# Kernel optimization log

Measured on AMD Instinct MI355X. Metric: run time of the kernel, lower is better.

## Reference

```python
import jax, jax.numpy as jnp
import numpy as np

B, T, IN, H, L = 32, 1024, 256, 256, 2  # batch, length, input_size, hidden_size, num_layers


def _lstm_scan(x, W_ih, W_hh, b_ih, b_hh, reverse):
    """Single-direction LSTM over time. x:[B,T,D] -> h:[B,T,H]. PyTorch gate order i,f,g,o."""
    b, t, _ = x.shape
    h_dim = W_hh.shape[1]
    # Precompute input contribution for all timesteps at once: [T,B,4H]
    xg = (jnp.einsum('btd,gd->btg', x, W_ih) + b_ih + b_hh).transpose(1, 0, 2)

    def step(carry, g_t):
        h, c = carry
        g = g_t + h @ W_hh.T
        i, f, gg, o = jnp.split(g, 4, axis=-1)
        c = jax.nn.sigmoid(f) * c + jax.nn.sigmoid(i) * jnp.tanh(gg)
        h = jax.nn.sigmoid(o) * jnp.tanh(c)
        return (h, c), h

    init = (jnp.zeros((b, h_dim), x.dtype), jnp.zeros((b, h_dim), x.dtype))
    _, hs = jax.lax.scan(step, init, xg, reverse=reverse)  # hs:[T,B,H], original time order
    return hs.transpose(1, 0, 2)


def setup_inputs() -> dict:
    key = jax.random.key(0)
    ks = iter(jax.random.split(key, 40))
    s = 1.0 / np.sqrt(H)
    inp = {'x': jax.random.normal(next(ks), (B, T, IN), jnp.float32)}
    for l in range(L):
        d_in = IN if l == 0 else 2 * H
        for dr in ('f', 'r'):
            inp[f'W_ih_{dr}{l}'] = jax.random.uniform(next(ks), (4 * H, d_in), jnp.float32, -s, s)
            inp[f'W_hh_{dr}{l}'] = jax.random.uniform(next(ks), (4 * H, H), jnp.float32, -s, s)
            inp[f'b_ih_{dr}{l}'] = jax.random.uniform(next(ks), (4 * H,), jnp.float32, -s, s)
            inp[f'b_hh_{dr}{l}'] = jax.random.uniform(next(ks), (4 * H,), jnp.float32, -s, s)
    return inp


def reference(x,
              W_ih_f0, W_hh_f0, b_ih_f0, b_hh_f0,
              W_ih_r0, W_hh_r0, b_ih_r0, b_hh_r0,
              W_ih_f1, W_hh_f1, b_ih_f1, b_hh_f1,
              W_ih_r1, W_hh_r1, b_ih_r1, b_hh_r1):
    fwd = [(W_ih_f0, W_hh_f0, b_ih_f0, b_hh_f0), (W_ih_f1, W_hh_f1, b_ih_f1, b_hh_f1)]
    rev = [(W_ih_r0, W_hh_r0, b_ih_r0, b_hh_r0), (W_ih_r1, W_hh_r1, b_ih_r1, b_hh_r1)]
    h = x
    for l in range(L):
        hf = _lstm_scan(h, *fwd[l], reverse=False)
        hr = _lstm_scan(h, *rev[l], reverse=True)
        h = jnp.concatenate([hf, hr], axis=-1)  # [B,T,2H]
    return h
```

## Files before the change

kernel.cpp:

```cpp
#include <hip/hip_runtime.h>
#include <hip/hip_fp16.h>


#define T_LEN 1024
#define BATCH 32
#define HID   256
#define G4    1024

struct __align__(16) Half8 { __half h[8]; };

typedef _Float16 f16x2 __attribute__((ext_vector_type(2)));
typedef _Float16 half8_t __attribute__((ext_vector_type(8)));
typedef float f32x4 __attribute__((ext_vector_type(4)));

__device__ __forceinline__ f16x2 pack_f16x2(float lo, float hi) {
    f16x2 r; r.x = (_Float16)lo; r.y = (_Float16)hi; return r;
}
__device__ __forceinline__ float dot2acc(f16x2 a, f16x2 b, float c) {
#if __has_builtin(__builtin_amdgcn_fdot2)
    return __builtin_amdgcn_fdot2(a, b, c, false);
#else
    return c + (float)a.x * (float)b.x + (float)a.y * (float)b.y;
#endif
}

template <int CTRL>
__device__ __forceinline__ unsigned qperm_u32(unsigned v) {
    int r = __builtin_amdgcn_update_dpp((int)v, (int)v, CTRL, 0xF, 0xF, true);
    return (unsigned)r;
}

__device__ __forceinline__ float sigm(float x) { return 1.0f / (1.0f + __expf(-x)); }
__device__ __forceinline__ float tanh_fast(float x) {
    float e = __expf(2.f * x);
    return 1.f - 2.f / (e + 1.f);
}

__global__ __launch_bounds__(256, 2) void proj_mfma(
    const float* __restrict__ A, int K,
    const float* __restrict__ Wf, const float* __restrict__ Wr,
    const float* __restrict__ bih_f, const float* __restrict__ bhh_f,
    const float* __restrict__ bih_r, const float* __restrict__ bhh_r,
    __half* __restrict__ xg)
{
    const int dir = blockIdx.z;
    const float* __restrict__ W   = dir ? Wr    : Wf;
    const float* __restrict__ bih = dir ? bih_r : bih_f;
    const float* __restrict__ bhh = dir ? bhh_r : bhh_f;
    __half* __restrict__ outp = xg + (size_t)dir * ((size_t)BATCH * T_LEN * G4);

    __shared__ char psm[36864];
    __half* As = (__half*)psm;
    __half* Bs = (__half*)(psm + 18432);

    const int tid  = threadIdx.x;
    const int lane = tid & 63;
    const int wave = tid >> 6;
    const int wm   = wave >> 1;
    const int wn   = wave & 1;
    const int fr   = lane & 15;
    const int fk   = lane >> 4;
    const int m0   = blockIdx.y * 128;
    const int n0   = blockIdx.x * 128;

    float biasv[4];
    #pragma unroll
    for (int ni = 0; ni < 4; ++ni) {
        int n = n0 + wn * 64 + ni * 16 + fr;
        biasv[ni] = bih[n] + bhh[n];
    }

    f32x4 acc[4][4];
    #pragma unroll
    for (int mi = 0; mi < 4; ++mi)
        #pragma unroll
        for (int ni = 0; ni < 4; ++ni)
            acc[mi][ni] = (f32x4){0.f, 0.f, 0.f, 0.f};

    for (int k0 = 0; k0 < K; k0 += 64) {
        #pragma unroll
        for (int it = 0; it < 4; ++it) {
            int t2  = tid + it * 256;
            int row = t2 >> 3;
            int ks  = (t2 & 7) * 8;
            const float* pa = &A[(size_t)(m0 + row) * K + k0 + ks];
            const float* pb = &W[(size_t)(n0 + row) * K + k0 + ks];
            float4 a0 = *reinterpret_cast<const float4*>(pa);
            float4 a1 = *reinterpret_cast<const float4*>(pa + 4);
            float4 b0 = *reinterpret_cast<const float4*>(pb);
            float4 b1 = *reinterpret_cast<const float4*>(pb + 4);
            Half8 ha, hb;
            ha.h[0] = __float2half(a0.x); ha.h[1] = __float2half(a0.y);
            ha.h[2] = __float2half(a0.z); ha.h[3] = __float2half(a0.w);
            ha.h[4] = __float2half(a1.x); ha.h[5] = __float2half(a1.y);
            ha.h[6] = __float2half(a1.z); ha.h[7] = __float2half(a1.w);
            hb.h[0] = __float2half(b0.x); hb.h[1] = __float2half(b0.y);
            hb.h[2] = __float2half(b0.z); hb.h[3] = __float2half(b0.w);
            hb.h[4] = __float2half(b1.x); hb.h[5] = __float2half(b1.y);
            hb.h[6] = __float2half(b1.z); hb.h[7] = __float2half(b1.w);
            *reinterpret_cast<Half8*>(&As[row * 72 + ks]) = ha;
            *reinterpret_cast<Half8*>(&Bs[row * 72 + ks]) = hb;
        }
        __syncthreads();

        #pragma unroll
        for (int kk = 0; kk < 2; ++kk) {
            half8_t af[4], bf[4];
            #pragma unroll
            for (int mi = 0; mi < 4; ++mi)
                af[mi] = *reinterpret_cast<const half8_t*>(
                    &As[(wm * 64 + mi * 16 + fr) * 72 + kk * 32 + fk * 8]);
            #pragma unroll
            for (int ni = 0; ni < 4; ++ni)
                bf[ni] = *reinterpret_cast<const half8_t*>(
                    &Bs[(wn * 64 + ni * 16 + fr) * 72 + kk * 32 + fk * 8]);
            #pragma unroll
            for (int mi = 0; mi < 4; ++mi)
                #pragma unroll
                for (int ni = 0; ni < 4; ++ni)
                    acc[mi][ni] = __builtin_amdgcn_mfma_f32_16x16x32_f16(
                        af[mi], bf[ni], acc[mi][ni], 0, 0, 0);
        }
        __syncthreads();
    }

    __half* Cs = (__half*)psm;
    #pragma unroll
    for (int mi = 0; mi < 4; ++mi)
        #pragma unroll
        for (int ni = 0; ni < 4; ++ni) {
            #pragma unroll
            for (int i = 0; i < 4; ++i) {
                int row = wm * 64 + mi * 16 + fk * 4 + i;
                int col = wn * 64 + ni * 16 + fr;
                Cs[row * 136 + col] = __float2half(acc[mi][ni][i] + biasv[ni]);
            }
        }
    __syncthreads();
    #pragma unroll
    for (int it = 0; it < 8; ++it) {
        int slot = it * 256 + tid;
        int row  = slot >> 4;
        int c8   = (slot & 15) * 8;
        Half8 v = *reinterpret_cast<const Half8*>(&Cs[row * 136 + c8]);
        *reinterpret_cast<Half8*>(&outp[(size_t)(m0 + row) * G4 + n0 + c8]) = v;
    }
}

extern "C" __global__ __launch_bounds__(512, 2) void recur12_kernel(
    const __half* __restrict__ xg,
    const float* __restrict__ Whh_f,
    const float* __restrict__ Whh_r,
    float* __restrict__ outp,
    unsigned long long* __restrict__ hbt,
    unsigned int tagbase)
{
    __shared__ char smem[55296];
    __half* hl  = (__half*)smem;
    float*  scr = (float*)(smem + 1024);

    const int tid = threadIdx.x;
    const int bid = blockIdx.x;
    const int jq  = bid >> 6;
    const int d   = (bid >> 5) & 1;
    const int b   = bid & 31;
    const float* __restrict__ Whh = d ? Whh_r : Whh_f;

    const int kh = tid >> 8;
    const int r  = tid & 255;
    const int q  = r >> 6;
    const int jl = r & 63;
    const int n_my = (q << 8) + jq * 64 + jl;

    unsigned wh[64];
    {
        const float* wrow = Whh + (size_t)n_my * HID + kh * 128;
        #pragma unroll
        for (int i = 0; i < 32; ++i) {
            float4 w4 = *reinterpret_cast<const float4*>(&wrow[i * 4]);
            wh[2 * i]     = __builtin_bit_cast(unsigned, pack_f16x2(w4.x, w4.y));
            wh[2 * i + 1] = __builtin_bit_cast(unsigned, pack_f16x2(w4.z, w4.w));
        }
    }
    #pragma unroll
    for (int i = 0; i < 64; ++i) asm volatile("" : "+v"(wh[i]));

    unsigned long long* hb = hbt + (size_t)(d * 32 + b) * 512;

    if (tid < 32) {
        __hip_atomic_store(&hb[256 + jq * 32 + tid],
                           (unsigned long long)tagbase << 32,
                           __ATOMIC_RELAXED, __HIP_MEMORY_SCOPE_AGENT);
    }
    if (tid < 64) hl[0 * 256 + jq * 64 + tid] = __float2half(0.f);

    const bool isPoll = (tid >= 256) && (tid < 352);
    int pslot = 0, pdst = 0;
    if (isPoll) {
        int u  = tid - 256;
        int fq = u >> 5;
        int qq = fq + (fq >= jq);
        int pi = u & 31;
        pslot  = qq * 32 + pi;
        pdst   = qq * 64 + pi * 2;
    }

    const __half* __restrict__ xgp =
        xg + ((size_t)(d * BATCH + b)) * T_LEN * G4 + n_my;

    float c_state = 0.f;

    for (int st = 0; st < T_LEN; ++st) {
        const int t = d ? (T_LEN - 1 - st) : st;

        float xv = (kh == 0) ? __half2float(xgp[(size_t)t * G4]) : 0.f;

        __half* hlcur = hl + (st & 1) * 256;

        if (isPoll) {
            const unsigned int exp = tagbase + (unsigned)st;
            unsigned long long* src = hb + (size_t)((st + 1) & 1) * 256 + pslot;
            unsigned long long v =
                __hip_atomic_load(src, __ATOMIC_RELAXED, __HIP_MEMORY_SCOPE_AGENT);
            while ((unsigned int)(v >> 32) != exp)
                v = __hip_atomic_load(src, __ATOMIC_RELAXED, __HIP_MEMORY_SCOPE_AGENT);
            *reinterpret_cast<unsigned*>(&hlcur[pdst]) = (unsigned)v;
        }
        __syncthreads();

        float a0 = xv, a1 = 0.f;
        {
            const float4* hp = reinterpret_cast<const float4*>(hlcur + kh * 128);
            #pragma unroll
            for (int i = 0; i < 16; ++i) {
                float4 hv = hp[i];
                a0 = dot2acc(__builtin_bit_cast(f16x2, hv.x), __builtin_bit_cast(f16x2, wh[4 * i + 0]), a0);
                a1 = dot2acc(__builtin_bit_cast(f16x2, hv.y), __builtin_bit_cast(f16x2, wh[4 * i + 1]), a1);
                a0 = dot2acc(__builtin_bit_cast(f16x2, hv.z), __builtin_bit_cast(f16x2, wh[4 * i + 2]), a0);
                a1 = dot2acc(__builtin_bit_cast(f16x2, hv.w), __builtin_bit_cast(f16x2, wh[4 * i + 3]), a1);
            }
        }
        scr[kh * 256 + r] = a0 + a1;
        __syncthreads();

        if (tid < 64) {
            float gi = scr[      tid] + scr[256 +       tid];
            float gf = scr[ 64 + tid] + scr[256 +  64 + tid];
            float gg = scr[128 + tid] + scr[256 + 128 + tid];
            float go = scr[192 + tid] + scr[256 + 192 + tid];
            float ii = sigm(gi);
            float ff = sigm(gf);
            float g2 = tanh_fast(gg);
            float oo = sigm(go);
            c_state = ff * c_state + ii * g2;
            float h = oo * tanh_fast(c_state);
            const int j = jq * 64 + tid;

            __half h16 = __float2half(h);
            hl[((st + 1) & 1) * 256 + j] = h16;

            unsigned hbits = (unsigned)__builtin_bit_cast(unsigned short, h16);
            unsigned nb = qperm_u32<0xB1>(hbits);
            if ((tid & 1) == 0) {
                unsigned payload = hbits | (nb << 16);
                unsigned long long pv =
                    ((unsigned long long)(tagbase + (unsigned)st + 1u) << 32) | payload;
                __hip_atomic_store(&hb[(size_t)(st & 1) * 256 + jq * 32 + (tid >> 1)], pv,
                                   __ATOMIC_RELAXED, __HIP_MEMORY_SCOPE_AGENT);
            }
            outp[((size_t)b * T_LEN + t) * (2 * HID) + d * HID + j] = h;
        }
    }
}

extern "C" void kernel_launch(void* const* d_in, const int* in_sizes, int n_in,
                              void* d_out, int out_size, void* d_ws, size_t ws_size,
                              hipStream_t stream)
{
    const float* x       = (const float*)d_in[0];
    const float* W_ih_f0 = (const float*)d_in[1];
    const float* W_hh_f0 = (const float*)d_in[2];
    const float* b_ih_f0 = (const float*)d_in[3];
    const float* b_hh_f0 = (const float*)d_in[4];
    const float* W_ih_r0 = (const float*)d_in[5];
    const float* W_hh_r0 = (const float*)d_in[6];
    const float* b_ih_r0 = (const float*)d_in[7];
    const float* b_hh_r0 = (const float*)d_in[8];
    const float* W_ih_f1 = (const float*)d_in[9];
    const float* W_hh_f1 = (const float*)d_in[10];
    const float* b_ih_f1 = (const float*)d_in[11];
    const float* b_hh_f1 = (const float*)d_in[12];
    const float* W_ih_r1 = (const float*)d_in[13];
    const float* W_hh_r1 = (const float*)d_in[14];
    const float* b_ih_r1 = (const float*)d_in[15];
    const float* b_hh_r1 = (const float*)d_in[16];

    float* outp = (float*)d_out;

    __half* xg = (__half*)d_ws;
    const size_t xg_bytes = (size_t)2 * BATCH * T_LEN * G4 * sizeof(__half);
    unsigned long long* hbt = (unsigned long long*)((char*)d_ws + xg_bytes);

    hipMemsetAsync(hbt, 0, 262144, stream);

    proj_mfma<<<dim3(8, 256, 2), 256, 0, stream>>>(x, 256, W_ih_f0, W_ih_r0,
        b_ih_f0, b_hh_f0, b_ih_r0, b_hh_r0, xg);
    {
        const __half* xg_c = xg;
        unsigned int base0 = 1u;
        void* args[] = {(void*)&xg_c, (void*)&W_hh_f0, (void*)&W_hh_r0,
                        (void*)&outp, (void*)&hbt, (void*)&base0};
        hipLaunchCooperativeKernel(reinterpret_cast<const void*>(recur12_kernel),
                                   dim3(256), dim3(512), args, 0, stream);
    }

    proj_mfma<<<dim3(8, 256, 2), 256, 0, stream>>>(outp, 512, W_ih_f1, W_ih_r1,
        b_ih_f1, b_hh_f1, b_ih_r1, b_hh_r1, xg);
    {
        const __half* xg_c = xg;
        unsigned int base1 = 4096u;
        void* args[] = {(void*)&xg_c, (void*)&W_hh_f1, (void*)&W_hh_r1,
                        (void*)&outp, (void*)&hbt, (void*)&base1};
        hipLaunchCooperativeKernel(reinterpret_cast<const void*>(recur12_kernel),
                                   dim3(256), dim3(512), args, 0, stream);
    }
}
```

Measured before the change: 2.923 ms.

## Interleave gate rows per cell and combine gates via DPP to drop a barrier

Restructures the recurrent kernel so each of 256 compute threads holds a full 256-wide W_hh row (128 packed registers), with the four gates of a cell in adjacent lanes. The gates are exchanged with DPP quad permutes instead of going through an LDS scratch buffer, which removes the second __syncthreads per timestep and the split-K reduction. The block shrinks to 384 threads: 256 compute plus poll threads, with compute given raised priority. It also requests 96KB of dynamic LDS, apparently to force one block per CU, at the cost of much higher register pressure per thread.

```diff
diff --git a/kernel.cpp b/kernel.cpp
--- a/kernel.cpp
+++ b/kernel.cpp
@@ -25,9 +25,10 @@
 }
 
 template <int CTRL>
-__device__ __forceinline__ unsigned qperm_u32(unsigned v) {
-    int r = __builtin_amdgcn_update_dpp((int)v, (int)v, CTRL, 0xF, 0xF, true);
-    return (unsigned)r;
+__device__ __forceinline__ float qpermf(float v) {
+    int i = __builtin_bit_cast(int, v);
+    int r = __builtin_amdgcn_update_dpp(i, i, CTRL, 0xF, 0xF, true);
+    return __builtin_bit_cast(float, r);
 }
 
 __device__ __forceinline__ float sigm(float x) { return 1.0f / (1.0f + __expf(-x)); }
@@ -35,6 +36,8 @@
     float e = __expf(2.f * x);
     return 1.f - 2.f / (e + 1.f);
 }
+
+#define WH(i) __builtin_bit_cast(f16x2, wh[i])
 
 __global__ __launch_bounds__(256, 2) void proj_mfma(
     const float* __restrict__ A, int K,
@@ -147,7 +150,7 @@
     }
 }
 
-extern "C" __global__ __launch_bounds__(512, 2) void recur12_kernel(
+extern "C" __global__ __launch_bounds__(384, 2) void recur15_kernel(
     const __half* __restrict__ xg,
     const float* __restrict__ Whh_f,
     const float* __restrict__ Whh_r,
@@ -155,9 +158,8 @@
     unsigned long long* __restrict__ hbt,
     unsigned int tagbase)
 {
-    __shared__ char smem[55296];
-    __half* hl  = (__half*)smem;
-    float*  scr = (float*)(smem + 1024);
+    extern __shared__ char smem[];
+    __half* hl = (__half*)smem;
 
     const int tid = threadIdx.x;
     const int bid = blockIdx.x;
@@ -166,24 +168,23 @@
     const int b   = bid & 31;
     const float* __restrict__ Whh = d ? Whh_r : Whh_f;
 
-    const int kh = tid >> 8;
-    const int r  = tid & 255;
-    const int q  = r >> 6;
-    const int jl = r & 63;
-    const int n_my = (q << 8) + jq * 64 + jl;
-
-    unsigned wh[64];
-    {
-        const float* wrow = Whh + (size_t)n_my * HID + kh * 128;
-        #pragma unroll
-        for (int i = 0; i < 32; ++i) {
+    const int jl = (tid >> 2) & 63;
+    const int q  = tid & 3;
+    const int cell_my = jq * 64 + jl;
+    const int n_my = (q << 8) + cell_my;
+
+    unsigned wh[128];
+    if (tid < 256) {
+        const float* wrow = Whh + (size_t)n_my * HID;
+        #pragma unroll
+        for (int i = 0; i < 64; ++i) {
             float4 w4 = *reinterpret_cast<const float4*>(&wrow[i * 4]);
             wh[2 * i]     = __builtin_bit_cast(unsigned, pack_f16x2(w4.x, w4.y));
             wh[2 * i + 1] = __builtin_bit_cast(unsigned, pack_f16x2(w4.z, w4.w));
         }
-    }
-    #pragma unroll
-    for (int i = 0; i < 64; ++i) asm volatile("" : "+v"(wh[i]));
+        #pragma unroll
+        for (int i = 0; i < 128; ++i) asm volatile("" : "+v"(wh[i]));
+    }
 
     unsigned long long* hb = hbt + (size_t)(d * 32 + b) * 512;
 
@@ -193,6 +194,7 @@
                            __ATOMIC_RELAXED, __HIP_MEMORY_SCOPE_AGENT);
     }
     if (tid < 64) hl[0 * 256 + jq * 64 + tid] = __float2half(0.f);
+    __syncthreads();
 
     const bool isPoll = (tid >= 256) && (tid < 352);
     int pslot = 0, pdst = 0;
@@ -212,66 +214,82 @@
 
     for (int st = 0; st < T_LEN; ++st) {
         const int t = d ? (T_LEN - 1 - st) : st;
-
-        float xv = (kh == 0) ? __half2float(xgp[(size_t)t * G4]) : 0.f;
-
-        __half* hlcur = hl + (st & 1) * 256;
+        const int par = st & 1;
 
         if (isPoll) {
-            const unsigned int exp = tagbase + (unsigned)st;
-            unsigned long long* src = hb + (size_t)((st + 1) & 1) * 256 + pslot;
+            const unsigned exp = tagbase + (unsigned)st;
+            unsigned long long* src = &hb[(size_t)((st + 1) & 1) * 256 + pslot];
             unsigned long long v =
                 __hip_atomic_load(src, __ATOMIC_RELAXED, __HIP_MEMORY_SCOPE_AGENT);
-            while ((unsigned int)(v >> 32) != exp)
+            while ((unsigned)(v >> 32) != exp)
                 v = __hip_atomic_load(src, __ATOMIC_RELAXED, __HIP_MEMORY_SCOPE_AGENT);
-            *reinterpret_cast<unsigned*>(&hlcur[pdst]) = (unsigned)v;
+            *reinterpret_cast<unsigned*>(&hl[par * 256 + pdst]) = (unsigned)v;
         }
         __syncthreads();
 
-        float a0 = xv, a1 = 0.f;
-        {
-            const float4* hp = reinterpret_cast<const float4*>(hlcur + kh * 128);
-            #pragma unroll
-            for (int i = 0; i < 16; ++i) {
-                float4 hv = hp[i];
-                a0 = dot2acc(__builtin_bit_cast(f16x2, hv.x), __builtin_bit_cast(f16x2, wh[4 * i + 0]), a0);
-                a1 = dot2acc(__builtin_bit_cast(f16x2, hv.y), __builtin_bit_cast(f16x2, wh[4 * i + 1]), a1);
-                a0 = dot2acc(__builtin_bit_cast(f16x2, hv.z), __builtin_bit_cast(f16x2, wh[4 * i + 2]), a0);
-                a1 = dot2acc(__builtin_bit_cast(f16x2, hv.w), __builtin_bit_cast(f16x2, wh[4 * i + 3]), a1);
+        if (tid < 256) {
+            __builtin_amdgcn_s_setprio(1);
+            float xv = __half2float(xgp[(size_t)t * G4]);
+            float a0 = 0.f, a1 = 0.f, a2 = 0.f, a3 = 0.f;
+            const float4* hp = reinterpret_cast<const float4*>(hl + par * 256);
+            #pragma unroll
+            for (int i = 0; i < 8; ++i) {
+                float4 h0 = hp[i];
+                float4 h1 = hp[8 + i];
+                float4 h2 = hp[16 + i];
+                float4 h3 = hp[24 + i];
+                a0 = dot2acc(__builtin_bit_cast(f16x2, h0.x), WH(4*i+0),   a0);
+                a0 = dot2acc(__builtin_bit_cast(f16x2, h0.y), WH(4*i+1),   a0);
+                a0 = dot2acc(__builtin_bit_cast(f16x2, h0.z), WH(4*i+2),   a0);
+                a0 = dot2acc(__builtin_bit_cast(f16x2, h0.w), WH(4*i+3),   a0);
+                a1 = dot2acc(__builtin_bit_cast(f16x2, h1.x), WH(32+4*i+0), a1);
+                a1 = dot2acc(__builtin_bit_cast(f16x2, h1.y), WH(32+4*i+1), a1);
+                a1 = dot2acc(__builtin_bit_cast(f16x2, h1.z), WH(32+4*i+2), a1);
+                a1 = dot2acc(__builtin_bit_cast(f16x2, h1.w), WH(32+4*i+3), a1);
+                a2 = dot2acc(__builtin_bit_cast(f16x2, h2.x), WH(64+4*i+0), a2);
+                a2 = dot2acc(__builtin_bit_cast(f16x2, h2.y), WH(64+4*i+1), a2);
+                a2 = dot2acc(__builtin_bit_cast(f16x2, h2.z), WH(64+4*i+2), a2);
+                a2 = dot2acc(__builtin_bit_cast(f16x2, h2.w), WH(64+4*i+3), a2);
+                a3 = dot2acc(__builtin_bit_cast(f16x2, h3.x), WH(96+4*i+0), a3);
+                a3 = dot2acc(__builtin_bit_cast(f16x2, h3.y), WH(96+4*i+1), a3);
+                a3 = dot2acc(__builtin_bit_cast(f16x2, h3.z), WH(96+4*i+2), a3);
+                a3 = dot2acc(__builtin_bit_cast(f16x2, h3.w), WH(96+4*i+3), a3);
             }
-        }
-        scr[kh * 256 + r] = a0 + a1;
-        __syncthreads();
-
-        if (tid < 64) {
-            float gi = scr[      tid] + scr[256 +       tid];
-            float gf = scr[ 64 + tid] + scr[256 +  64 + tid];
-            float gg = scr[128 + tid] + scr[256 + 128 + tid];
-            float go = scr[192 + tid] + scr[256 + 192 + tid];
-            float ii = sigm(gi);
-            float ff = sigm(gf);
-            float g2 = tanh_fast(gg);
-            float oo = sigm(go);
+            float v = ((a0 + a1) + (a2 + a3)) + xv;
+
+            float x1 = qpermf<0xB1>(v);
+            float x2 = qpermf<0x4E>(v);
+            float x3 = qpermf<0xB1>(x2);
+
+            float ii = sigm(v);
+            float ff = sigm(x1);
+            float g2 = tanh_fast(x2);
+            float oo = sigm(x3);
             c_state = ff * c_state + ii * g2;
             float h = oo * tanh_fast(c_state);
-            const int j = jq * 64 + tid;
-
-            __half h16 = __float2half(h);
-            hl[((st + 1) & 1) * 256 + j] = h16;
-
-            unsigned hbits = (unsigned)__builtin_bit_cast(unsigned short, h16);
-            unsigned nb = qperm_u32<0xB1>(hbits);
-            if ((tid & 1) == 0) {
-                unsigned payload = hbits | (nb << 16);
-                unsigned long long pv =
-                    ((unsigned long long)(tagbase + (unsigned)st + 1u) << 32) | payload;
-                __hip_atomic_store(&hb[(size_t)(st & 1) * 256 + jq * 32 + (tid >> 1)], pv,
-                                   __ATOMIC_RELAXED, __HIP_MEMORY_SCOPE_AGENT);
+
+            float hpart = __shfl_down(h, 4);
+
+            if (q == 0) {
+                __half h16 = __float2half(h);
+                hl[(par ^ 1) * 256 + cell_my] = h16;
+                if ((jl & 1) == 0) {
+                    unsigned payload =
+                        (unsigned)__builtin_bit_cast(unsigned short, h16) |
+                        ((unsigned)__builtin_bit_cast(unsigned short, __float2half(hpart)) << 16);
+                    unsigned long long pv =
+                        ((unsigned long long)(tagbase + (unsigned)st + 1u) << 32) | payload;
+                    __hip_atomic_store(&hb[(size_t)par * 256 + jq * 32 + (jl >> 1)], pv,
+                                       __ATOMIC_RELAXED, __HIP_MEMORY_SCOPE_AGENT);
+                }
+                outp[((size_t)b * T_LEN + t) * (2 * HID) + d * HID + cell_my] = h;
             }
-            outp[((size_t)b * T_LEN + t) * (2 * HID) + d * HID + j] = h;
-        }
-    }
-}
+            __builtin_amdgcn_s_setprio(0);
+        }
+    }
+}
+
+#define RECUR_LDS 98304u
 
 extern "C" void kernel_launch(void* const* d_in, const int* in_sizes, int n_in,
                               void* d_out, int out_size, void* d_ws, size_t ws_size,
@@ -301,6 +319,9 @@
     const size_t xg_bytes = (size_t)2 * BATCH * T_LEN * G4 * sizeof(__half);
     unsigned long long* hbt = (unsigned long long*)((char*)d_ws + xg_bytes);
 
+    hipFuncSetAttribute(reinterpret_cast<const void*>(recur15_kernel),
+                        hipFuncAttributeMaxDynamicSharedMemorySize, RECUR_LDS);
+
     hipMemsetAsync(hbt, 0, 262144, stream);
 
     proj_mfma<<<dim3(8, 256, 2), 256, 0, stream>>>(x, 256, W_ih_f0, W_ih_r0,
@@ -310,8 +331,8 @@
         unsigned int base0 = 1u;
         void* args[] = {(void*)&xg_c, (void*)&W_hh_f0, (void*)&W_hh_r0,
                         (void*)&outp, (void*)&hbt, (void*)&base0};
-        hipLaunchCooperativeKernel(reinterpret_cast<const void*>(recur12_kernel),
-                                   dim3(256), dim3(512), args, 0, stream);
+        hipLaunchCooperativeKernel(reinterpret_cast<const void*>(recur15_kernel),
+                                   dim3(256), dim3(384), args, RECUR_LDS, stream);
     }
 
     proj_mfma<<<dim3(8, 256, 2), 256, 0, stream>>>(outp, 512, W_ih_f1, W_ih_r1,
@@ -321,7 +342,7 @@
         unsigned int base1 = 4096u;
         void* args[] = {(void*)&xg_c, (void*)&W_hh_f1, (void*)&W_hh_r1,
                         (void*)&outp, (void*)&hbt, (void*)&base1};
-        hipLaunchCooperativeKernel(reinterpret_cast<const void*>(recur12_kernel),
-                                   dim3(256), dim3(512), args, 0, stream);
-    }
-}
+        hipLaunchCooperativeKernel(reinterpret_cast<const void*>(recur15_kernel),
+                                   dim3(256), dim3(384), args, RECUR_LDS, stream);
+    }
+}
```

Result: slower. 3.629 ms (+24.1%).
